# Optimization experiments

Measured on AMD Instinct MI355X. Metric: run time of the kernel, lower is better.

## Reference

```python
import jax, jax.numpy as jnp
import numpy as np

D_MODEL = 1024
N_HEADS = 16
D_HEAD = 64
TOTAL = N_HEADS * D_HEAD


def setup_inputs() -> dict:
    key = jax.random.key(0)
    k1, k2, k3 = jax.random.split(key, 3)
    x = jax.random.normal(k1, (2, 2048, D_MODEL), dtype=jnp.float32)
    W_qkv = jax.random.normal(k2, (3 * TOTAL, D_MODEL), dtype=jnp.float32) * 0.02
    W_out = jax.random.normal(k3, (D_MODEL, TOTAL), dtype=jnp.float32) * 0.02
    return {"x": x, "W_qkv": W_qkv, "W_out": W_out}


def reference(x, W_qkv, W_out):
    B, T, D = x.shape
    scale = D_HEAD ** -0.5
    qkv = jnp.einsum('btd,ed->bte', x, W_qkv)  # [B,T,3*TOTAL]
    q, k, v = jnp.split(qkv, 3, axis=-1)
    def heads(t):
        return t.reshape(B, T, N_HEADS, D_HEAD).transpose(0, 2, 1, 3)  # [B,H,T,Dh]
    q, k, v = heads(q), heads(k), heads(v)
    scores = jnp.einsum('bhqd,bhkd->bhqk', q, k) * scale
    causal = jnp.tril(jnp.ones((T, T), dtype=bool))
    scores = jnp.where(causal[None, None], scores, -jnp.inf)
    attn = jax.nn.softmax(scores, axis=-1)
    out = jnp.einsum('bhqk,bhkd->bhqd', attn, v)
    out = out.transpose(0, 2, 1, 3).reshape(B, T, TOTAL)
    return jnp.einsum('bte,de->btd', out, W_out)
```

## Files before the change

### kernel.cpp

```cpp
#include <hip/hip_runtime.h>
#include <hip/hip_bf16.h>

typedef __attribute__((ext_vector_type(4))) float f32x4;
typedef __attribute__((ext_vector_type(8))) short s16x8;
typedef __attribute__((ext_vector_type(4))) short s16x4;

#define DEV static __device__ __forceinline__

DEV unsigned short f2bf(float f) {
    unsigned int u = __builtin_bit_cast(unsigned int, f);
    u += 0x7fffu + ((u >> 16) & 1u);
    return (unsigned short)(u >> 16);
}

#if __has_builtin(__builtin_amdgcn_exp2f)
#define EXP2(x) __builtin_amdgcn_exp2f(x)
#else
#define EXP2(x) exp2f(x)
#endif

DEV unsigned int pack2(float a, float b) {
#if __has_builtin(__builtin_amdgcn_perm)
    return __builtin_amdgcn_perm(__builtin_bit_cast(unsigned int, b),
                                 __builtin_bit_cast(unsigned int, a), 0x07060302u);
#else
    return (__builtin_bit_cast(unsigned int, a) >> 16) |
           (__builtin_bit_cast(unsigned int, b) & 0xffff0000u);
#endif
}

DEV s16x8 ld8(const unsigned short* p) {
    s16x4 lo = *(const s16x4*)(p);
    s16x4 hi = *(const s16x4*)(p + 4);
    return __builtin_shufflevector(lo, hi, 0, 1, 2, 3, 4, 5, 6, 7);
}
DEV s16x8 ld8a(const unsigned short* p) { return *(const s16x8*)p; }

DEV f32x4 mfma16(s16x8 a, s16x8 b, f32x4 c) {
    return __builtin_amdgcn_mfma_f32_16x16x32_bf16(a, b, c, 0, 0, 0);
}

DEV void glds16(const unsigned short* g, unsigned short* l) {
    __builtin_amdgcn_global_load_lds(
        (const __attribute__((address_space(1))) unsigned int*)g,
        (__attribute__((address_space(3))) unsigned int*)l, 16, 0, 0);
}

__global__ __launch_bounds__(256) void convf2b3(
        const float* __restrict__ s0, unsigned short* __restrict__ d0, int n40,
        const float* __restrict__ s1, unsigned short* __restrict__ d1, int n41,
        const float* __restrict__ s2, unsigned short* __restrict__ d2, int n42) {
    int i = blockIdx.x * 256 + threadIdx.x;
    if (i < n40) {
        float4 v = ((const float4*)s0)[i];
        s16x4 o = {(short)f2bf(v.x), (short)f2bf(v.y), (short)f2bf(v.z), (short)f2bf(v.w)};
        ((s16x4*)d0)[i] = o;
    } else if (i - n40 < n41) {
        int j = i - n40;
        float4 v = ((const float4*)s1)[j];
        s16x4 o = {(short)f2bf(v.x), (short)f2bf(v.y), (short)f2bf(v.z), (short)f2bf(v.w)};
        ((s16x4*)d1)[j] = o;
    } else if (i - n40 - n41 < n42) {
        int j = i - n40 - n41;
        float4 v = ((const float4*)s2)[j];
        s16x4 o = {(short)f2bf(v.x), (short)f2bf(v.y), (short)f2bf(v.z), (short)f2bf(v.w)};
        ((s16x4*)d2)[j] = o;
    }
}

__global__ __launch_bounds__(256) void convf2b(const float* __restrict__ s,
                                               unsigned short* __restrict__ d, int n4) {
    int i = blockIdx.x * 256 + threadIdx.x;
    if (i < n4) {
        float4 v = ((const float4*)s)[i];
        s16x4 o = {(short)f2bf(v.x), (short)f2bf(v.y), (short)f2bf(v.z), (short)f2bf(v.w)};
        ((s16x4*)d)[i] = o;
    }
}

__global__ __launch_bounds__(512) void qkv_gemm(
        const unsigned short* __restrict__ Xb, const unsigned short* __restrict__ Wq,
        unsigned short* __restrict__ q_ws, unsigned short* __restrict__ k_ws,
        unsigned short* __restrict__ v_ws) {
    __shared__ unsigned short As[2][128 * 32];
    __shared__ unsigned short Bs[2][128 * 32];
    const int tid = threadIdx.x, lane = tid & 63, wave = tid >> 6;
    const int l15 = lane & 15, l4 = lane >> 4;
    const int wm = (wave >> 1) * 32, wn = (wave & 1) * 64;
    const int m0 = blockIdx.y * 128, n0 = blockIdx.x * 128;

    f32x4 acc[2][4];
    for (int i = 0; i < 2; i++)
        for (int j = 0; j < 4; j++) acc[i][j] = (f32x4){0.f, 0.f, 0.f, 0.f};

    const unsigned short* aptr = &Xb[(size_t)(m0 + wave * 16 + (lane >> 2)) * 1024 + (lane & 3) * 8];
    const unsigned short* bptr = &Wq[(size_t)(n0 + wave * 16 + (lane >> 2)) * 1024 + (lane & 3) * 8];

    for (int k0 = 0; k0 < 1024; k0 += 64) {
        __syncthreads();
        for (int c = 0; c < 2; c++) {
            glds16(aptr + k0 + c * 32, &As[c][(wave * 16) * 32]);
            glds16(bptr + k0 + c * 32, &Bs[c][(wave * 16) * 32]);
        }
        __syncthreads();
        for (int c = 0; c < 2; c++) {
            s16x8 af[2], bf[4];
            for (int mt = 0; mt < 2; mt++) af[mt] = ld8a(&As[c][(wm + mt * 16 + l15) * 32 + l4 * 8]);
            for (int nt = 0; nt < 4; nt++) bf[nt] = ld8a(&Bs[c][(wn + nt * 16 + l15) * 32 + l4 * 8]);
            for (int mt = 0; mt < 2; mt++)
                for (int nt = 0; nt < 4; nt++)
                    acc[mt][nt] = mfma16(af[mt], bf[nt], acc[mt][nt]);
        }
    }

    const int gnb = n0 + wn;
    const int which = gnb >> 10, h = (gnb >> 6) & 15;
    const int bidx = m0 >> 11, tb = m0 & 2047;
    if (which == 2) {
        unsigned short* dst = v_ws + (size_t)(bidx * 16 + h) * 64 * 2048;
        for (int mt = 0; mt < 2; mt++) {
            int t = tb + wm + mt * 16 + l4 * 4;
            for (int nt = 0; nt < 4; nt++) {
                int dh = nt * 16 + l15;
                s16x4 pp;
                for (int r = 0; r < 4; r++) pp[r] = (short)f2bf(acc[mt][nt][r]);
                *(s16x4*)&dst[(size_t)dh * 2048 + t] = pp;
            }
        }
    } else {
        unsigned short* dst = ((which == 0) ? q_ws : k_ws) + (size_t)(bidx * 16 + h) * 2048 * 64;
        const float sc = (which == 0) ? 0.18033688f : 1.0f;
        for (int mt = 0; mt < 2; mt++) {
            int t0 = tb + wm + mt * 16 + l4 * 4;
            for (int nt = 0; nt < 4; nt++) {
                int dh = nt * 16 + l15;
                for (int r = 0; r < 4; r++)
                    dst[(size_t)(t0 + r) * 64 + dh] = f2bf(acc[mt][nt][r] * sc);
            }
        }
    }
}

__global__ __launch_bounds__(512, 2) void attn(
        const unsigned short* __restrict__ q_ws, const unsigned short* __restrict__ k_ws,
        const unsigned short* __restrict__ v_ws, unsigned short* __restrict__ ao) {
    constexpr int LDP = 68;
    __shared__ unsigned short Ks[3][2][64 * 32];
    __shared__ unsigned short Vt[3][2][64 * 32];
    __shared__ unsigned short Ps[8 * 32 * LDP];
    const int tid = threadIdx.x, lane = tid & 63, wave = tid >> 6;
    const int l15 = lane & 15, l4 = lane >> 4;
    const int xf = (l15 >> 1) & 3;

    const int id = blockIdx.x;
    const int bh8 = id & 7, rest = id >> 3;
    const int p = rest & 7, g = rest >> 3;
    const int bh = bh8 + 8 * g, b = bh >> 4, h = bh & 15;
    const int chunk = (wave < 4) ? (15 - p) : p;
    const int qrow = chunk * 128 + (wave & 3) * 32;
    const int nt = 2 * (16 - p);

    const size_t base = (size_t)bh * 2048 * 64;
    const unsigned short* vtb = v_ws + (size_t)bh * 64 * 2048;
    unsigned short* Pw = &Ps[wave * 32 * LDP];

    const int seg = wave >> 1, hf = wave & 1;
    const int srow = lane >> 2;
    const int scol = ((lane & 3) ^ ((lane >> 3) & 3)) * 8;
    const unsigned short* kg = &k_ws[base + (size_t)(seg * 16 + srow) * 64 + hf * 32 + scol];
    const unsigned short* vg = &vtb[(size_t)(seg * 16 + srow) * 2048 + hf * 32 + scol];
    unsigned short* kld = &Ks[0][hf][(seg * 16) * 32];
    unsigned short* vld = &Vt[0][hf][(seg * 16) * 32];
    const unsigned short* krd = &Ks[0][0][0];
    const unsigned short* vrd = &Vt[0][0][0];

    s16x8 qf[2][2];
#pragma unroll
    for (int qs = 0; qs < 2; qs++)
#pragma unroll
        for (int c = 0; c < 2; c++)
            qf[qs][c] = ld8a(&q_ws[base + (size_t)(qrow + qs * 16 + l15) * 64 + c * 32 + l4 * 8]);
    asm volatile("s_waitcnt vmcnt(0)" ::: "memory");

    f32x4 o[2][4];
#pragma unroll
    for (int qs = 0; qs < 2; qs++)
#pragma unroll
        for (int i = 0; i < 4; i++) o[qs][i] = (f32x4){0.f, 0.f, 0.f, 0.f};
    float lsum[2] = {0.f, 0.f};

    glds16(kg, kld);
    glds16(vg, vld);
    glds16(kg + 4096, kld + 4096);
    glds16(vg + 64, vld + 4096);

    int cur = 0;
    for (int r = 0; r < nt; ++r) {
        if (r + 1 < nt) asm volatile("s_waitcnt vmcnt(2)" ::: "memory");
        else            asm volatile("s_waitcnt vmcnt(0)" ::: "memory");
        __builtin_amdgcn_s_barrier();
        if (r + 2 < nt) {
            const int nb = (cur == 0) ? 2 : cur - 1;
            glds16(kg + (size_t)(r + 2) * 4096, kld + nb * 4096);
            glds16(vg + (r + 2) * 64,           vld + nb * 4096);
        }
        const int k0 = r * 64;
        if (k0 < qrow + 16) {
            const unsigned short* kb = krd + cur * 4096;
            const unsigned short* vb = vrd + cur * 4096;
            f32x4 st[2][4];
#pragma unroll
            for (int qs = 0; qs < 2; qs++)
#pragma unroll
                for (int ks = 0; ks < 4; ks++) st[qs][ks] = (f32x4){0.f, 0.f, 0.f, 0.f};
            __builtin_amdgcn_s_setprio(1);
#pragma unroll
            for (int c = 0; c < 2; c++)
#pragma unroll
                for (int ks = 0; ks < 4; ks++) {
                    s16x8 kf = ld8a(&kb[c * 2048 + (ks * 16 + l15) * 32 + (l4 ^ xf) * 8]);
                    st[0][ks] = mfma16(kf, qf[0][c], st[0][ks]);
                    st[1][ks] = mfma16(kf, qf[1][c], st[1][ks]);
                }
            __builtin_amdgcn_s_setprio(0);

#pragma unroll
            for (int qs = 0; qs < 2; qs++) {
                const int qb = qrow + qs * 16;
                if (k0 + 63 > qb) {
                    int qg = qb + l15;
#pragma unroll
                    for (int ks = 0; ks < 4; ks++)
#pragma unroll
                        for (int rr = 0; rr < 4; rr++) {
                            int kgi = k0 + ks * 16 + l4 * 4 + rr;
                            if (kgi > qg) st[qs][ks][rr] = -1e30f;
                        }
                }
                float part = 0.f;
#pragma unroll
                for (int ks = 0; ks < 4; ks++) {
                    float p0 = EXP2(st[qs][ks][0]);
                    float p1 = EXP2(st[qs][ks][1]);
                    float p2 = EXP2(st[qs][ks][2]);
                    float p3 = EXP2(st[qs][ks][3]);
                    part += (p0 + p1) + (p2 + p3);
                    unsigned int u0 = pack2(p0, p1), u1 = pack2(p2, p3);
                    *(uint2*)&Pw[(qs * 16 + l15) * LDP + ks * 16 + l4 * 4] = (uint2){u0, u1};
                }
                lsum[qs] += part;
            }

            s16x8 pf[2][2];
#pragma unroll
            for (int qs = 0; qs < 2; qs++)
#pragma unroll
                for (int c = 0; c < 2; c++)
                    pf[qs][c] = ld8(&Pw[(qs * 16 + l15) * LDP + c * 32 + l4 * 8]);
            __builtin_amdgcn_s_setprio(1);
#pragma unroll
            for (int c = 0; c < 2; c++)
#pragma unroll
                for (int ds = 0; ds < 4; ds++) {
                    s16x8 vf = ld8a(&vb[c * 2048 + (ds * 16 + l15) * 32 + (l4 ^ xf) * 8]);
                    o[0][ds] = mfma16(vf, pf[0][c], o[0][ds]);
                    o[1][ds] = mfma16(vf, pf[1][c], o[1][ds]);
                }
            __builtin_amdgcn_s_setprio(0);
        }
        cur = (cur == 2) ? 0 : cur + 1;
    }

#pragma unroll
    for (int qs = 0; qs < 2; qs++) {
        float t = lsum[qs];
        t += __shfl_xor(t, 16, 64);
        t += __shfl_xor(t, 32, 64);
        float inv = 1.f / t;
#pragma unroll
        for (int ds = 0; ds < 4; ds++) {
            s16x4 pp;
#pragma unroll
            for (int r = 0; r < 4; r++) pp[r] = (short)f2bf(o[qs][ds][r] * inv);
            *(s16x4*)&Pw[(qs * 16 + l15) * LDP + ds * 16 + l4 * 4] = pp;
        }
    }
    int qr = lane >> 2, qt = lane & 3;
#pragma unroll
    for (int qs = 0; qs < 2; qs++) {
        size_t orow = ((size_t)b * 2048 + qrow + qs * 16 + qr) * 1024 + h * 64 + qt * 16;
        *(s16x8*)&ao[orow]     = ld8(&Pw[(qs * 16 + qr) * LDP + qt * 16]);
        *(s16x8*)&ao[orow + 8] = ld8(&Pw[(qs * 16 + qr) * LDP + qt * 16 + 8]);
    }
}

__global__ __launch_bounds__(256) void out_gemm(
        const unsigned short* __restrict__ A, const unsigned short* __restrict__ Bm,
        float* __restrict__ OUT) {
    __shared__ unsigned short As[2][128 * 32];
    __shared__ unsigned short Bs[2][64 * 32];
    const int tid = threadIdx.x, lane = tid & 63, wave = tid >> 6;
    const int l15 = lane & 15, l4 = lane >> 4;
    const int wm = wave * 32;
    const int m0 = blockIdx.y * 128, n0 = blockIdx.x * 64;

    f32x4 acc[2][4];
    for (int i = 0; i < 2; i++)
        for (int j = 0; j < 4; j++) acc[i][j] = (f32x4){0.f, 0.f, 0.f, 0.f};

    const unsigned short* aptr = &A[(size_t)(m0 + wave * 32 + (lane >> 2)) * 1024 + (lane & 3) * 8];
    const unsigned short* bptr = &Bm[(size_t)(n0 + wave * 16 + (lane >> 2)) * 1024 + (lane & 3) * 8];

    for (int k0 = 0; k0 < 1024; k0 += 64) {
        __syncthreads();
        for (int c = 0; c < 2; c++) {
            glds16(aptr + k0 + c * 32, &As[c][(wave * 32) * 32]);
            glds16(aptr + k0 + c * 32 + 16 * 1024, &As[c][(wave * 32 + 16) * 32]);
            glds16(bptr + k0 + c * 32, &Bs[c][(wave * 16) * 32]);
        }
        __syncthreads();
        for (int c = 0; c < 2; c++) {
            s16x8 af[2], bf[4];
            for (int mt = 0; mt < 2; mt++) af[mt] = ld8a(&As[c][(wm + mt * 16 + l15) * 32 + l4 * 8]);
            for (int nt = 0; nt < 4; nt++) bf[nt] = ld8a(&Bs[c][(nt * 16 + l15) * 32 + l4 * 8]);
            for (int mt = 0; mt < 2; mt++)
                for (int nt = 0; nt < 4; nt++)
                    acc[mt][nt] = mfma16(af[mt], bf[nt], acc[mt][nt]);
        }
    }

    for (int mt = 0; mt < 2; mt++)
        for (int nt = 0; nt < 4; nt++)
            for (int r = 0; r < 4; r++) {
                int gm = m0 + wm + mt * 16 + l4 * 4 + r;
                int gn = n0 + nt * 16 + l15;
                OUT[(size_t)gm * 1024 + gn] = acc[mt][nt][r];
            }
}

extern "C" void kernel_launch(void* const* d_in, const int* in_sizes, int n_in,
                              void* d_out, int out_size, void* d_ws, size_t ws_size,
                              hipStream_t stream) {
    (void)in_sizes; (void)n_in; (void)out_size;
    const float* x    = (const float*)d_in[0];
    const float* Wqkv = (const float*)d_in[1];
    const float* Wout = (const float*)d_in[2];
    float* out = (float*)d_out;

    unsigned short* q_ws = (unsigned short*)d_ws;
    unsigned short* k_ws = q_ws + (size_t)4 * 1024 * 1024;
    unsigned short* v_ws = k_ws + (size_t)4 * 1024 * 1024;
    unsigned short* xb   = v_ws + (size_t)4 * 1024 * 1024;
    unsigned short* ao   = xb;
    unsigned short* wqb  = (unsigned short*)d_out;

    const int n4x = 2 * 2048 * 1024 / 4, n4w = 3072 * 1024 / 4, n4o = 1024 * 1024 / 4;
    const bool merged = ws_size >= (size_t)35 * 1024 * 1024;
    unsigned short* wob = merged ? (q_ws + (size_t)16 * 1024 * 1024)
                                 : q_ws;

    if (merged) {
        convf2b3<<<(n4x + n4w + n4o + 255) / 256, 256, 0, stream>>>(
            x, xb, n4x, Wqkv, wqb, n4w, Wout, wob, n4o);
    } else {
        convf2b3<<<(n4x + n4w + 255) / 256, 256, 0, stream>>>(
            x, xb, n4x, Wqkv, wqb, n4w, Wout, wob, 0);
    }
    qkv_gemm<<<dim3(24, 32), 512, 0, stream>>>(xb, wqb, q_ws, k_ws, v_ws);
    attn<<<dim3(256), 512, 0, stream>>>(q_ws, k_ws, v_ws, ao);
    if (!merged) convf2b<<<1024, 256, 0, stream>>>(Wout, wob, n4o);
    out_gemm<<<dim3(16, 32), 256, 0, stream>>>(ao, wob, out);
}
```

Before: 175.4 us.

## Split high query chunk's KV range across both wave groups with merged partial outputs

The attention block is restructured so that the four waves handling the low query chunk, once they finish their short causal range, take over the tail of the high chunk's key/value range. Each wave group now stages its own K/V tiles into separate LDS buffers, and the loop is fixed at 17 iterations instead of 2*(16-p). Partial outputs and row sums for the high chunk are merged through LDS before the epilogue. The intent is to even out per-wave work and shorten the block's critical path. In exchange it doubles the K/V staging traffic and LDS use (about 130KB), which may lower occupancy below the two blocks per CU the launch bounds request.

```diff
diff --git a/kernel.cpp b/kernel.cpp
--- a/kernel.cpp
+++ b/kernel.cpp
@@ -145,9 +145,13 @@
         const unsigned short* __restrict__ q_ws, const unsigned short* __restrict__ k_ws,
         const unsigned short* __restrict__ v_ws, unsigned short* __restrict__ ao) {
     constexpr int LDP = 68;
-    __shared__ unsigned short Ks[3][2][64 * 32];
-    __shared__ unsigned short Vt[3][2][64 * 32];
-    __shared__ unsigned short Ps[8 * 32 * LDP];
+    __shared__ unsigned short lds[66560];
+    unsigned short* KsA = lds;
+    unsigned short* VtA = lds + 12288;
+    unsigned short* KsB = lds + 24576;
+    unsigned short* VtB = lds + 36864;
+    unsigned short* Ps  = lds + 49152;
+
     const int tid = threadIdx.x, lane = tid & 63, wave = tid >> 6;
     const int l15 = lane & 15, l4 = lane >> 4;
     const int xf = (l15 >> 1) & 3;
@@ -156,141 +160,193 @@
     const int bh8 = id & 7, rest = id >> 3;
     const int p = rest & 7, g = rest >> 3;
     const int bh = bh8 + 8 * g, b = bh >> 4, h = bh & 15;
-    const int chunk = (wave < 4) ? (15 - p) : p;
-    const int qrow = chunk * 128 + (wave & 3) * 32;
-    const int nt = 2 * (16 - p);
+    const bool isA = wave < 4;
+    const int w4 = wave & 3;
+    const int qrow_hi = (15 - p) * 128 + w4 * 32;
+    const int qrow_lo = p * 128 + w4 * 32;
+    const int Tlo = 2 * p + 2;
 
     const size_t base = (size_t)bh * 2048 * 64;
     const unsigned short* vtb = v_ws + (size_t)bh * 64 * 2048;
     unsigned short* Pw = &Ps[wave * 32 * LDP];
 
-    const int seg = wave >> 1, hf = wave & 1;
-    const int srow = lane >> 2;
+    const int seg = w4, srow = lane >> 2;
     const int scol = ((lane & 3) ^ ((lane >> 3) & 3)) * 8;
-    const unsigned short* kg = &k_ws[base + (size_t)(seg * 16 + srow) * 64 + hf * 32 + scol];
-    const unsigned short* vg = &vtb[(size_t)(seg * 16 + srow) * 2048 + hf * 32 + scol];
-    unsigned short* kld = &Ks[0][hf][(seg * 16) * 32];
-    unsigned short* vld = &Vt[0][hf][(seg * 16) * 32];
-    const unsigned short* krd = &Ks[0][0][0];
-    const unsigned short* vrd = &Vt[0][0][0];
-
-    s16x8 qf[2][2];
+    const unsigned short* kg = &k_ws[base + (size_t)(seg * 16 + srow) * 64 + scol];
+    const unsigned short* vg = &vtb[(size_t)(seg * 16 + srow) * 2048 + scol];
+    unsigned short* Ksm = isA ? KsA : KsB;
+    unsigned short* Vtm = isA ? VtA : VtB;
+
+    auto stage = [&](int tau, int buf) {
+        const unsigned short* kgt = kg + (size_t)tau * 4096;
+        const unsigned short* vgt = vg + tau * 64;
+        unsigned short* kd = Ksm + buf * 4096 + seg * 512;
+        unsigned short* vd = Vtm + buf * 4096 + seg * 512;
+        glds16(kgt,      kd);
+        glds16(kgt + 32, kd + 2048);
+        glds16(vgt,      vd);
+        glds16(vgt + 32, vd + 2048);
+    };
+    auto myTile = [&](int x) { return (isA || x < Tlo) ? x : 17 + x - Tlo; };
+
+    s16x8 qfh[2][2], qfl[2][2];
 #pragma unroll
     for (int qs = 0; qs < 2; qs++)
 #pragma unroll
         for (int c = 0; c < 2; c++)
-            qf[qs][c] = ld8a(&q_ws[base + (size_t)(qrow + qs * 16 + l15) * 64 + c * 32 + l4 * 8]);
+            qfh[qs][c] = ld8a(&q_ws[base + (size_t)(qrow_hi + qs * 16 + l15) * 64 + c * 32 + l4 * 8]);
+    if (!isA) {
+#pragma unroll
+        for (int qs = 0; qs < 2; qs++)
+#pragma unroll
+            for (int c = 0; c < 2; c++)
+                qfl[qs][c] = ld8a(&q_ws[base + (size_t)(qrow_lo + qs * 16 + l15) * 64 + c * 32 + l4 * 8]);
+    }
     asm volatile("s_waitcnt vmcnt(0)" ::: "memory");
 
-    f32x4 o[2][4];
+    f32x4 oh[2][4], ol[2][4];
+    float lh[2] = {0.f, 0.f}, ll[2] = {0.f, 0.f};
 #pragma unroll
     for (int qs = 0; qs < 2; qs++)
 #pragma unroll
-        for (int i = 0; i < 4; i++) o[qs][i] = (f32x4){0.f, 0.f, 0.f, 0.f};
-    float lsum[2] = {0.f, 0.f};
-
-    glds16(kg, kld);
-    glds16(vg, vld);
-    glds16(kg + 4096, kld + 4096);
-    glds16(vg + 64, vld + 4096);
-
-    int cur = 0;
-    for (int r = 0; r < nt; ++r) {
-        if (r + 1 < nt) asm volatile("s_waitcnt vmcnt(2)" ::: "memory");
-        else            asm volatile("s_waitcnt vmcnt(0)" ::: "memory");
+        for (int i = 0; i < 4; i++) {
+            oh[qs][i] = (f32x4){0.f, 0.f, 0.f, 0.f};
+            ol[qs][i] = (f32x4){0.f, 0.f, 0.f, 0.f};
+        }
+
+    auto compute = [&](const unsigned short* kb, const unsigned short* vb,
+                       s16x8 (&qf)[2][2], f32x4 (&o)[2][4], float (&ls)[2],
+                       int qrow, int k0) {
+        f32x4 st[2][4];
+#pragma unroll
+        for (int qs = 0; qs < 2; qs++)
+#pragma unroll
+            for (int ks = 0; ks < 4; ks++) st[qs][ks] = (f32x4){0.f, 0.f, 0.f, 0.f};
+        __builtin_amdgcn_s_setprio(1);
+#pragma unroll
+        for (int c = 0; c < 2; c++)
+#pragma unroll
+            for (int ks = 0; ks < 4; ks++) {
+                s16x8 kf = ld8a(&kb[c * 2048 + (ks * 16 + l15) * 32 + (l4 ^ xf) * 8]);
+                st[0][ks] = mfma16(kf, qf[0][c], st[0][ks]);
+                st[1][ks] = mfma16(kf, qf[1][c], st[1][ks]);
+            }
+        __builtin_amdgcn_s_setprio(0);
+
+#pragma unroll
+        for (int qs = 0; qs < 2; qs++) {
+            const int qb = qrow + qs * 16;
+            if (k0 + 63 > qb) {
+                int qg = qb + l15;
+#pragma unroll
+                for (int ks = 0; ks < 4; ks++)
+#pragma unroll
+                    for (int rr = 0; rr < 4; rr++) {
+                        int kgi = k0 + ks * 16 + l4 * 4 + rr;
+                        if (kgi > qg) st[qs][ks][rr] = -1e30f;
+                    }
+            }
+            float part = 0.f;
+#pragma unroll
+            for (int ks = 0; ks < 4; ks++) {
+                float p0 = EXP2(st[qs][ks][0]);
+                float p1 = EXP2(st[qs][ks][1]);
+                float p2 = EXP2(st[qs][ks][2]);
+                float p3 = EXP2(st[qs][ks][3]);
+                part += (p0 + p1) + (p2 + p3);
+                unsigned int u0 = pack2(p0, p1), u1 = pack2(p2, p3);
+                *(uint2*)&Pw[(qs * 16 + l15) * LDP + ks * 16 + l4 * 4] = (uint2){u0, u1};
+            }
+            ls[qs] += part;
+        }
+
+        s16x8 pf[2][2];
+#pragma unroll
+        for (int qs = 0; qs < 2; qs++)
+#pragma unroll
+            for (int c = 0; c < 2; c++)
+                pf[qs][c] = ld8(&Pw[(qs * 16 + l15) * LDP + c * 32 + l4 * 8]);
+        __builtin_amdgcn_s_setprio(1);
+#pragma unroll
+        for (int c = 0; c < 2; c++)
+#pragma unroll
+            for (int ds = 0; ds < 4; ds++) {
+                s16x8 vf = ld8a(&vb[c * 2048 + (ds * 16 + l15) * 32 + (l4 ^ xf) * 8]);
+                o[0][ds] = mfma16(vf, pf[0][c], o[0][ds]);
+                o[1][ds] = mfma16(vf, pf[1][c], o[1][ds]);
+            }
+        __builtin_amdgcn_s_setprio(0);
+    };
+
+    stage(myTile(0), 0);
+    stage(myTile(1), 1);
+
+    for (int r = 0; r < 17; ++r) {
+        if (r < 16) asm volatile("s_waitcnt vmcnt(4)" ::: "memory");
+        else        asm volatile("s_waitcnt vmcnt(0)" ::: "memory");
         __builtin_amdgcn_s_barrier();
-        if (r + 2 < nt) {
-            const int nb = (cur == 0) ? 2 : cur - 1;
-            glds16(kg + (size_t)(r + 2) * 4096, kld + nb * 4096);
-            glds16(vg + (r + 2) * 64,           vld + nb * 4096);
-        }
-        const int k0 = r * 64;
-        if (k0 < qrow + 16) {
-            const unsigned short* kb = krd + cur * 4096;
-            const unsigned short* vb = vrd + cur * 4096;
-            f32x4 st[2][4];
-#pragma unroll
-            for (int qs = 0; qs < 2; qs++)
-#pragma unroll
-                for (int ks = 0; ks < 4; ks++) st[qs][ks] = (f32x4){0.f, 0.f, 0.f, 0.f};
-            __builtin_amdgcn_s_setprio(1);
-#pragma unroll
-            for (int c = 0; c < 2; c++)
-#pragma unroll
-                for (int ks = 0; ks < 4; ks++) {
-                    s16x8 kf = ld8a(&kb[c * 2048 + (ks * 16 + l15) * 32 + (l4 ^ xf) * 8]);
-                    st[0][ks] = mfma16(kf, qf[0][c], st[0][ks]);
-                    st[1][ks] = mfma16(kf, qf[1][c], st[1][ks]);
-                }
-            __builtin_amdgcn_s_setprio(0);
-
-#pragma unroll
-            for (int qs = 0; qs < 2; qs++) {
-                const int qb = qrow + qs * 16;
-                if (k0 + 63 > qb) {
-                    int qg = qb + l15;
-#pragma unroll
-                    for (int ks = 0; ks < 4; ks++)
-#pragma unroll
-                        for (int rr = 0; rr < 4; rr++) {
-                            int kgi = k0 + ks * 16 + l4 * 4 + rr;
-                            if (kgi > qg) st[qs][ks][rr] = -1e30f;
-                        }
-                }
-                float part = 0.f;
-#pragma unroll
-                for (int ks = 0; ks < 4; ks++) {
-                    float p0 = EXP2(st[qs][ks][0]);
-                    float p1 = EXP2(st[qs][ks][1]);
-                    float p2 = EXP2(st[qs][ks][2]);
-                    float p3 = EXP2(st[qs][ks][3]);
-                    part += (p0 + p1) + (p2 + p3);
-                    unsigned int u0 = pack2(p0, p1), u1 = pack2(p2, p3);
-                    *(uint2*)&Pw[(qs * 16 + l15) * LDP + ks * 16 + l4 * 4] = (uint2){u0, u1};
-                }
-                lsum[qs] += part;
-            }
-
-            s16x8 pf[2][2];
-#pragma unroll
-            for (int qs = 0; qs < 2; qs++)
-#pragma unroll
-                for (int c = 0; c < 2; c++)
-                    pf[qs][c] = ld8(&Pw[(qs * 16 + l15) * LDP + c * 32 + l4 * 8]);
-            __builtin_amdgcn_s_setprio(1);
-#pragma unroll
-            for (int c = 0; c < 2; c++)
-#pragma unroll
-                for (int ds = 0; ds < 4; ds++) {
-                    s16x8 vf = ld8a(&vb[c * 2048 + (ds * 16 + l15) * 32 + (l4 ^ xf) * 8]);
-                    o[0][ds] = mfma16(vf, pf[0][c], o[0][ds]);
-                    o[1][ds] = mfma16(vf, pf[1][c], o[1][ds]);
-                }
-            __builtin_amdgcn_s_setprio(0);
-        }
-        cur = (cur == 2) ? 0 : cur + 1;
-    }
-
-#pragma unroll
-    for (int qs = 0; qs < 2; qs++) {
-        float t = lsum[qs];
-        t += __shfl_xor(t, 16, 64);
-        t += __shfl_xor(t, 32, 64);
-        float inv = 1.f / t;
-#pragma unroll
-        for (int ds = 0; ds < 4; ds++) {
-            s16x4 pp;
-#pragma unroll
-            for (int r = 0; r < 4; r++) pp[r] = (short)f2bf(o[qs][ds][r] * inv);
-            *(s16x4*)&Pw[(qs * 16 + l15) * LDP + ds * 16 + l4 * 4] = pp;
-        }
-    }
-    int qr = lane >> 2, qt = lane & 3;
-#pragma unroll
-    for (int qs = 0; qs < 2; qs++) {
-        size_t orow = ((size_t)b * 2048 + qrow + qs * 16 + qr) * 1024 + h * 64 + qt * 16;
-        *(s16x8*)&ao[orow]     = ld8(&Pw[(qs * 16 + qr) * LDP + qt * 16]);
-        *(s16x8*)&ao[orow + 8] = ld8(&Pw[(qs * 16 + qr) * LDP + qt * 16 + 8]);
+        if (r + 2 < 17) stage(myTile(r + 2), (r + 2) % 3);
+        const unsigned short* kb = Ksm + (r % 3) * 4096;
+        const unsigned short* vb = Vtm + (r % 3) * 4096;
+        if (isA) {
+            compute(kb, vb, qfh, oh, lh, qrow_hi, r * 64);
+        } else if (r < Tlo) {
+            if (r * 64 < qrow_lo + 16) compute(kb, vb, qfl, ol, ll, qrow_lo, r * 64);
+        } else {
+            const int k0 = (17 + r - Tlo) * 64;
+            if (k0 < qrow_hi + 16) compute(kb, vb, qfh, oh, lh, qrow_hi, k0);
+        }
+    }
+
+    __syncthreads();
+    float* mrg = (float*)lds;
+    f32x4* m4 = (f32x4*)mrg;
+    if (!isA) {
+#pragma unroll
+        for (int qs = 0; qs < 2; qs++) {
+#pragma unroll
+            for (int ds = 0; ds < 4; ds++)
+                m4[w4 * 544 + (qs * 4 + ds) * 64 + lane] = oh[qs][ds];
+            mrg[w4 * 2176 + 2048 + qs * 64 + lane] = lh[qs];
+        }
+    }
+    __syncthreads();
+
+    auto epilogue = [&](f32x4 (&o)[2][4], float (&ls)[2], int qrow) {
+#pragma unroll
+        for (int qs = 0; qs < 2; qs++) {
+            float t = ls[qs];
+            t += __shfl_xor(t, 16, 64);
+            t += __shfl_xor(t, 32, 64);
+            float inv = 1.f / t;
+#pragma unroll
+            for (int ds = 0; ds < 4; ds++) {
+                s16x4 pp;
+#pragma unroll
+                for (int r = 0; r < 4; r++) pp[r] = (short)f2bf(o[qs][ds][r] * inv);
+                *(s16x4*)&Pw[(qs * 16 + l15) * LDP + ds * 16 + l4 * 4] = pp;
+            }
+        }
+        int qr = lane >> 2, qt = lane & 3;
+#pragma unroll
+        for (int qs = 0; qs < 2; qs++) {
+            size_t orow = ((size_t)b * 2048 + qrow + qs * 16 + qr) * 1024 + h * 64 + qt * 16;
+            *(s16x8*)&ao[orow]     = ld8(&Pw[(qs * 16 + qr) * LDP + qt * 16]);
+            *(s16x8*)&ao[orow + 8] = ld8(&Pw[(qs * 16 + qr) * LDP + qt * 16 + 8]);
+        }
+    };
+
+    if (isA) {
+#pragma unroll
+        for (int qs = 0; qs < 2; qs++) {
+#pragma unroll
+            for (int ds = 0; ds < 4; ds++)
+                oh[qs][ds] += m4[w4 * 544 + (qs * 4 + ds) * 64 + lane];
+            lh[qs] += mrg[w4 * 2176 + 2048 + qs * 64 + lane];
+        }
+        epilogue(oh, lh, qrow_hi);
+    } else {
+        epilogue(ol, ll, qrow_lo);
     }
 }
 
```

After: 165.6 us. -5.6%, faster.

## Split attention into 256-thread blocks per query chunk and retile output GEMM

Applied to the files above, without the earlier changes.

The attention kernel moves from 512-thread blocks, each pairing a long and a short causal chunk, to 256-thread blocks that each handle one 128-row query chunk. Chunks are ordered longest first so the scheduler can balance load dynamically. K/V staging goes from triple to double buffering with a full vmcnt wait each step, which gives up some load/compute overlap. The per-wave P scratch becomes a smaller XOR-swizzled 16x64 tile that is reused per query subtile. The output GEMM is retiled from 128x64 to 64x128 blocks with a 2x2 wave layout.

```diff
diff --git a/kernel.cpp b/kernel.cpp
--- a/kernel.cpp
+++ b/kernel.cpp
@@ -141,73 +141,70 @@
     }
 }
 
-__global__ __launch_bounds__(512, 2) void attn(
+__global__ __launch_bounds__(256, 4) void attn(
         const unsigned short* __restrict__ q_ws, const unsigned short* __restrict__ k_ws,
         const unsigned short* __restrict__ v_ws, unsigned short* __restrict__ ao) {
-    constexpr int LDP = 68;
-    __shared__ unsigned short Ks[3][2][64 * 32];
-    __shared__ unsigned short Vt[3][2][64 * 32];
-    __shared__ unsigned short Ps[8 * 32 * LDP];
+    __shared__ unsigned short Ks[2][2][64 * 32];
+    __shared__ unsigned short Vt[2][2][64 * 32];
+    __shared__ unsigned short Ps[4 * 16 * 64];
     const int tid = threadIdx.x, lane = tid & 63, wave = tid >> 6;
     const int l15 = lane & 15, l4 = lane >> 4;
     const int xf = (l15 >> 1) & 3;
+    const int sw = (l15 & 7) << 3;
 
     const int id = blockIdx.x;
     const int bh8 = id & 7, rest = id >> 3;
-    const int p = rest & 7, g = rest >> 3;
+    const int g = rest & 3, ord = rest >> 2;
     const int bh = bh8 + 8 * g, b = bh >> 4, h = bh & 15;
-    const int chunk = (wave < 4) ? (15 - p) : p;
-    const int qrow = chunk * 128 + (wave & 3) * 32;
-    const int nt = 2 * (16 - p);
+    const int c = 15 - ord;
+    const int qrow = c * 128 + wave * 32;
+    const int T = 2 * c + 2;
 
     const size_t base = (size_t)bh * 2048 * 64;
     const unsigned short* vtb = v_ws + (size_t)bh * 64 * 2048;
-    unsigned short* Pw = &Ps[wave * 32 * LDP];
-
-    const int seg = wave >> 1, hf = wave & 1;
-    const int srow = lane >> 2;
+    unsigned short* Pw = &Ps[wave * 1024];
+
+    const int seg = wave, srow = lane >> 2;
     const int scol = ((lane & 3) ^ ((lane >> 3) & 3)) * 8;
-    const unsigned short* kg = &k_ws[base + (size_t)(seg * 16 + srow) * 64 + hf * 32 + scol];
-    const unsigned short* vg = &vtb[(size_t)(seg * 16 + srow) * 2048 + hf * 32 + scol];
-    unsigned short* kld = &Ks[0][hf][(seg * 16) * 32];
-    unsigned short* vld = &Vt[0][hf][(seg * 16) * 32];
-    const unsigned short* krd = &Ks[0][0][0];
-    const unsigned short* vrd = &Vt[0][0][0];
+    const unsigned short* kg = &k_ws[base + (size_t)(seg * 16 + srow) * 64 + scol];
+    const unsigned short* vg = &vtb[(size_t)(seg * 16 + srow) * 2048 + scol];
+
+    auto stage = [&](int tau, int buf) {
+        const unsigned short* kgt = kg + (size_t)tau * 4096;
+        const unsigned short* vgt = vg + tau * 64;
+        unsigned short* kd = &Ks[buf][0][seg * 512];
+        unsigned short* vd = &Vt[buf][0][seg * 512];
+        glds16(kgt,      kd);
+        glds16(kgt + 32, kd + 2048);
+        glds16(vgt,      vd);
+        glds16(vgt + 32, vd + 2048);
+    };
 
     s16x8 qf[2][2];
 #pragma unroll
     for (int qs = 0; qs < 2; qs++)
 #pragma unroll
-        for (int c = 0; c < 2; c++)
-            qf[qs][c] = ld8a(&q_ws[base + (size_t)(qrow + qs * 16 + l15) * 64 + c * 32 + l4 * 8]);
+        for (int c2 = 0; c2 < 2; c2++)
+            qf[qs][c2] = ld8a(&q_ws[base + (size_t)(qrow + qs * 16 + l15) * 64 + c2 * 32 + l4 * 8]);
     asm volatile("s_waitcnt vmcnt(0)" ::: "memory");
 
     f32x4 o[2][4];
+    float lsum[2] = {0.f, 0.f};
 #pragma unroll
     for (int qs = 0; qs < 2; qs++)
 #pragma unroll
         for (int i = 0; i < 4; i++) o[qs][i] = (f32x4){0.f, 0.f, 0.f, 0.f};
-    float lsum[2] = {0.f, 0.f};
-
-    glds16(kg, kld);
-    glds16(vg, vld);
-    glds16(kg + 4096, kld + 4096);
-    glds16(vg + 64, vld + 4096);
-
-    int cur = 0;
-    for (int r = 0; r < nt; ++r) {
-        if (r + 1 < nt) asm volatile("s_waitcnt vmcnt(2)" ::: "memory");
-        else            asm volatile("s_waitcnt vmcnt(0)" ::: "memory");
+
+    stage(0, 0);
+    for (int r = 0; r < T; ++r) {
+        asm volatile("s_waitcnt vmcnt(0)" ::: "memory");
         __builtin_amdgcn_s_barrier();
-        if (r + 2 < nt) {
-            const int nb = (cur == 0) ? 2 : cur - 1;
-            glds16(kg + (size_t)(r + 2) * 4096, kld + nb * 4096);
-            glds16(vg + (r + 2) * 64,           vld + nb * 4096);
-        }
+        if (r + 1 < T) stage(r + 1, (r + 1) & 1);
         const int k0 = r * 64;
-        if (k0 < qrow + 16) {
-            const unsigned short* kb = krd + cur * 4096;
-            const unsigned short* vb = vrd + cur * 4096;
+        if (k0 < qrow + 32) {
+            const unsigned short* kb = &Ks[r & 1][0][0];
+            const unsigned short* vb = &Vt[r & 1][0][0];
+
             f32x4 st[2][4];
 #pragma unroll
             for (int qs = 0; qs < 2; qs++)
@@ -215,15 +212,16 @@
                 for (int ks = 0; ks < 4; ks++) st[qs][ks] = (f32x4){0.f, 0.f, 0.f, 0.f};
             __builtin_amdgcn_s_setprio(1);
 #pragma unroll
-            for (int c = 0; c < 2; c++)
+            for (int c2 = 0; c2 < 2; c2++)
 #pragma unroll
                 for (int ks = 0; ks < 4; ks++) {
-                    s16x8 kf = ld8a(&kb[c * 2048 + (ks * 16 + l15) * 32 + (l4 ^ xf) * 8]);
-                    st[0][ks] = mfma16(kf, qf[0][c], st[0][ks]);
-                    st[1][ks] = mfma16(kf, qf[1][c], st[1][ks]);
+                    s16x8 kf = ld8a(&kb[c2 * 2048 + (ks * 16 + l15) * 32 + (l4 ^ xf) * 8]);
+                    st[0][ks] = mfma16(kf, qf[0][c2], st[0][ks]);
+                    st[1][ks] = mfma16(kf, qf[1][c2], st[1][ks]);
                 }
             __builtin_amdgcn_s_setprio(0);
 
+            s16x8 pf[2][2];
 #pragma unroll
             for (int qs = 0; qs < 2; qs++) {
                 const int qb = qrow + qs * 16;
@@ -246,31 +244,29 @@
                     float p3 = EXP2(st[qs][ks][3]);
                     part += (p0 + p1) + (p2 + p3);
                     unsigned int u0 = pack2(p0, p1), u1 = pack2(p2, p3);
-                    *(uint2*)&Pw[(qs * 16 + l15) * LDP + ks * 16 + l4 * 4] = (uint2){u0, u1};
+                    *(uint2*)&Pw[l15 * 64 + ((ks * 16 + l4 * 4) ^ sw)] = (uint2){u0, u1};
                 }
                 lsum[qs] += part;
+#pragma unroll
+                for (int c2 = 0; c2 < 2; c2++)
+                    pf[qs][c2] = ld8(&Pw[l15 * 64 + ((c2 * 32 + l4 * 8) ^ sw)]);
             }
 
-            s16x8 pf[2][2];
-#pragma unroll
-            for (int qs = 0; qs < 2; qs++)
-#pragma unroll
-                for (int c = 0; c < 2; c++)
-                    pf[qs][c] = ld8(&Pw[(qs * 16 + l15) * LDP + c * 32 + l4 * 8]);
             __builtin_amdgcn_s_setprio(1);
 #pragma unroll
-            for (int c = 0; c < 2; c++)
+            for (int c2 = 0; c2 < 2; c2++)
 #pragma unroll
                 for (int ds = 0; ds < 4; ds++) {
-                    s16x8 vf = ld8a(&vb[c * 2048 + (ds * 16 + l15) * 32 + (l4 ^ xf) * 8]);
-                    o[0][ds] = mfma16(vf, pf[0][c], o[0][ds]);
-                    o[1][ds] = mfma16(vf, pf[1][c], o[1][ds]);
+                    s16x8 vf = ld8a(&vb[c2 * 2048 + (ds * 16 + l15) * 32 + (l4 ^ xf) * 8]);
+                    o[0][ds] = mfma16(vf, pf[0][c2], o[0][ds]);
+                    o[1][ds] = mfma16(vf, pf[1][c2], o[1][ds]);
                 }
             __builtin_amdgcn_s_setprio(0);
         }
-        cur = (cur == 2) ? 0 : cur + 1;
-    }
-
+    }
+
+    int qr = lane >> 2, qt = lane & 3;
+    const int swr = (qr & 7) << 3;
 #pragma unroll
     for (int qs = 0; qs < 2; qs++) {
         float t = lsum[qs];
@@ -282,47 +278,43 @@
             s16x4 pp;
 #pragma unroll
             for (int r = 0; r < 4; r++) pp[r] = (short)f2bf(o[qs][ds][r] * inv);
-            *(s16x4*)&Pw[(qs * 16 + l15) * LDP + ds * 16 + l4 * 4] = pp;
-        }
-    }
-    int qr = lane >> 2, qt = lane & 3;
-#pragma unroll
-    for (int qs = 0; qs < 2; qs++) {
+            *(s16x4*)&Pw[l15 * 64 + ((ds * 16 + l4 * 4) ^ sw)] = pp;
+        }
         size_t orow = ((size_t)b * 2048 + qrow + qs * 16 + qr) * 1024 + h * 64 + qt * 16;
-        *(s16x8*)&ao[orow]     = ld8(&Pw[(qs * 16 + qr) * LDP + qt * 16]);
-        *(s16x8*)&ao[orow + 8] = ld8(&Pw[(qs * 16 + qr) * LDP + qt * 16 + 8]);
+        *(s16x8*)&ao[orow]     = ld8(&Pw[qr * 64 + ((qt * 16) ^ swr)]);
+        *(s16x8*)&ao[orow + 8] = ld8(&Pw[qr * 64 + ((qt * 16 + 8) ^ swr)]);
     }
 }
 
 __global__ __launch_bounds__(256) void out_gemm(
         const unsigned short* __restrict__ A, const unsigned short* __restrict__ Bm,
         float* __restrict__ OUT) {
-    __shared__ unsigned short As[2][128 * 32];
-    __shared__ unsigned short Bs[2][64 * 32];
+    __shared__ unsigned short As[2][64 * 32];
+    __shared__ unsigned short Bs[2][128 * 32];
     const int tid = threadIdx.x, lane = tid & 63, wave = tid >> 6;
     const int l15 = lane & 15, l4 = lane >> 4;
-    const int wm = wave * 32;
-    const int m0 = blockIdx.y * 128, n0 = blockIdx.x * 64;
+    const int wm = (wave >> 1) * 32, wn = (wave & 1) * 64;
+    const int m0 = blockIdx.y * 64, n0 = blockIdx.x * 128;
 
     f32x4 acc[2][4];
     for (int i = 0; i < 2; i++)
         for (int j = 0; j < 4; j++) acc[i][j] = (f32x4){0.f, 0.f, 0.f, 0.f};
 
-    const unsigned short* aptr = &A[(size_t)(m0 + wave * 32 + (lane >> 2)) * 1024 + (lane & 3) * 8];
-    const unsigned short* bptr = &Bm[(size_t)(n0 + wave * 16 + (lane >> 2)) * 1024 + (lane & 3) * 8];
+    const unsigned short* aptr = &A[(size_t)(m0 + wave * 16 + (lane >> 2)) * 1024 + (lane & 3) * 8];
+    const unsigned short* bptr = &Bm[(size_t)(n0 + wave * 32 + (lane >> 2)) * 1024 + (lane & 3) * 8];
 
     for (int k0 = 0; k0 < 1024; k0 += 64) {
         __syncthreads();
         for (int c = 0; c < 2; c++) {
-            glds16(aptr + k0 + c * 32, &As[c][(wave * 32) * 32]);
-            glds16(aptr + k0 + c * 32 + 16 * 1024, &As[c][(wave * 32 + 16) * 32]);
-            glds16(bptr + k0 + c * 32, &Bs[c][(wave * 16) * 32]);
+            glds16(aptr + k0 + c * 32, &As[c][(wave * 16) * 32]);
+            glds16(bptr + k0 + c * 32, &Bs[c][(wave * 32) * 32]);
+            glds16(bptr + k0 + c * 32 + 16 * 1024, &Bs[c][(wave * 32 + 16) * 32]);
         }
         __syncthreads();
         for (int c = 0; c < 2; c++) {
             s16x8 af[2], bf[4];
             for (int mt = 0; mt < 2; mt++) af[mt] = ld8a(&As[c][(wm + mt * 16 + l15) * 32 + l4 * 8]);
-            for (int nt = 0; nt < 4; nt++) bf[nt] = ld8a(&Bs[c][(nt * 16 + l15) * 32 + l4 * 8]);
+            for (int nt = 0; nt < 4; nt++) bf[nt] = ld8a(&Bs[c][(wn + nt * 16 + l15) * 32 + l4 * 8]);
             for (int mt = 0; mt < 2; mt++)
                 for (int nt = 0; nt < 4; nt++)
                     acc[mt][nt] = mfma16(af[mt], bf[nt], acc[mt][nt]);
@@ -333,7 +325,7 @@
         for (int nt = 0; nt < 4; nt++)
             for (int r = 0; r < 4; r++) {
                 int gm = m0 + wm + mt * 16 + l4 * 4 + r;
-                int gn = n0 + nt * 16 + l15;
+                int gn = n0 + wn + nt * 16 + l15;
                 OUT[(size_t)gm * 1024 + gn] = acc[mt][nt][r];
             }
 }
@@ -367,7 +359,7 @@
             x, xb, n4x, Wqkv, wqb, n4w, Wout, wob, 0);
     }
     qkv_gemm<<<dim3(24, 32), 512, 0, stream>>>(xb, wqb, q_ws, k_ws, v_ws);
-    attn<<<dim3(256), 512, 0, stream>>>(q_ws, k_ws, v_ws, ao);
+    attn<<<dim3(512), 256, 0, stream>>>(q_ws, k_ws, v_ws, ao);
     if (!merged) convf2b<<<1024, 256, 0, stream>>>(Wout, wob, n4o);
-    out_gemm<<<dim3(16, 32), 256, 0, stream>>>(ao, wob, out);
-}
+    out_gemm<<<dim3(8, 64), 256, 0, stream>>>(ao, wob, out);
+}
```

Result: no change. 174.6 us (-0.5%).
